# Kernel tuning notes

Measured on AMD Instinct MI355X. Metric: run time of the kernel, lower is better.

Reference implementation:

```python
import jax, jax.numpy as jnp
import numpy as np

B, S, H = 4, 2048, 576
NH, NKV, HD = 9, 3, 64
NEG = -1e9


def rotate_half(x):
    x1, x2 = x[..., : HD // 2], x[..., HD // 2 :]
    return jnp.concatenate((-x2, x1), axis=-1)


def setup_inputs() -> dict:
    key = jax.random.key(0)
    ks = jax.random.split(key, 6)
    x = jax.random.normal(ks[0], (B, S, H), dtype=jnp.float32)
    # realistic RoPE tables
    inv_freq = 1.0 / (10000.0 ** (np.arange(0, HD, 2, dtype=np.float32) / HD))
    pos = np.arange(S, dtype=np.float32)
    freqs = np.outer(pos, inv_freq)            # [S, HD//2]
    emb = np.concatenate([freqs, freqs], -1)   # [S, HD]
    cos = jnp.asarray(np.cos(emb), dtype=jnp.float32)
    sin = jnp.asarray(np.sin(emb), dtype=jnp.float32)
    # causal additive mask [1,1,S,S]
    causal = jnp.tril(jnp.ones((S, S), dtype=jnp.bool_))
    mask = jnp.where(causal, 0.0, NEG).astype(jnp.float32)[None, None]
    sc = 1.0 / np.sqrt(H)
    Wq = jax.random.normal(ks[1], (H, NH * HD), dtype=jnp.float32) * sc
    Wk = jax.random.normal(ks[2], (H, NKV * HD), dtype=jnp.float32) * sc
    Wv = jax.random.normal(ks[3], (H, NKV * HD), dtype=jnp.float32) * sc
    Wo = jax.random.normal(ks[4], (NH * HD, H), dtype=jnp.float32) * sc
    return {"x": x, "cos": cos, "sin": sin, "mask": mask,
            "Wq": Wq, "Wk": Wk, "Wv": Wv, "Wo": Wo}


def reference(x, cos, sin, mask, Wq, Wk, Wv, Wo):
    b, s, _ = x.shape
    # projections -> [b, heads, s, hd]
    q = (x @ Wq).reshape(b, s, NH, HD).transpose(0, 2, 1, 3)
    k = (x @ Wk).reshape(b, s, NKV, HD).transpose(0, 2, 1, 3)
    v = (x @ Wv).reshape(b, s, NKV, HD).transpose(0, 2, 1, 3)
    c = cos[None, None]  # [1,1,s,hd]
    sn = sin[None, None]
    q = q * c + rotate_half(q) * sn
    k = k * c + rotate_half(k) * sn
    # GQA: repeat_interleave KV heads to match query heads
    groups = NH // NKV
    k = jnp.repeat(k, groups, axis=1)
    v = jnp.repeat(v, groups, axis=1)
    scores = jnp.einsum("bhqd,bhkd->bhqk", q, k) / np.sqrt(HD)
    scores = scores + mask
    probs = jax.nn.softmax(scores, axis=-1)
    out = jnp.einsum("bhqk,bhkd->bhqd", probs, v)
    out = out.transpose(0, 2, 1, 3).reshape(b, s, NH * HD)
    return out @ Wo
```

## Files before the change

### kernel.cpp

```cpp
#include <hip/hip_runtime.h>
#include <math.h>

typedef __attribute__((ext_vector_type(4))) float f32x4;
typedef __attribute__((ext_vector_type(8))) short short8;
typedef __attribute__((ext_vector_type(8))) __bf16 bf16x8;
typedef __attribute__((ext_vector_type(2))) __bf16 bf16x2;
typedef __attribute__((ext_vector_type(2))) unsigned uint32x2;

#define NB 4
#define NS 2048
#define NHID 576
#define NHEADS 9
#define NKVH 3
#define NHD 64
#define NM (NB * NS)
#define NQKV 960
#define NGRP 3
#define QSC 0.18033688f

static __device__ __forceinline__ unsigned short f2bf(float f) {
  union { float f; unsigned u; } v; v.f = f;
  unsigned r = v.u + 0x7FFFu + ((v.u >> 16) & 1u);
  return (unsigned short)(r >> 16);
}
static __device__ __forceinline__ unsigned pk2bf(float a, float b) {
  bf16x2 h;
  h.x = (__bf16)a;
  h.y = (__bf16)b;
  return __builtin_bit_cast(unsigned, h);
}
static __device__ __forceinline__ f32x4 mfma16(short8 a, short8 b, f32x4 c) {
  return __builtin_amdgcn_mfma_f32_16x16x32_bf16(
      __builtin_bit_cast(bf16x8, a), __builtin_bit_cast(bf16x8, b), c, 0, 0, 0);
}
static __device__ __forceinline__ void gload16(const void* g, void* l) {
  __builtin_amdgcn_global_load_lds(
      (const __attribute__((address_space(1))) void*)g,
      (__attribute__((address_space(3))) void*)l, 16, 0, 0);
}

__global__ __launch_bounds__(256)
void k_cvt(const float* __restrict__ src, unsigned short* __restrict__ dst, const int n8) {
  const int t = blockIdx.x * 256 + threadIdx.x;
  if (t >= n8) return;
  const f32x4* sp = (const f32x4*)(src + (size_t)t * 8);
  f32x4 a = sp[0], b = sp[1];
  union { short8 v; unsigned short u[8]; } o;
#pragma unroll
  for (int e = 0; e < 4; ++e) { o.u[e] = f2bf(a[e]); o.u[4 + e] = f2bf(b[e]); }
  *(short8*)(dst + (size_t)t * 8) = o.v;
}

__global__ __launch_bounds__(256)
void k_transpose_cvt(const float* __restrict__ src, unsigned short* __restrict__ dst,
                     const int R, const int C) {
  __shared__ unsigned short tile[64 * 72];
  const int t = threadIdx.x;
  const int r0 = blockIdx.y * 64, c0 = blockIdx.x * 64;
  {
    const int rl = t >> 2, cb = (t & 3) * 16;
    const float* sp = src + (size_t)(r0 + rl) * C + c0 + cb;
#pragma unroll
    for (int jj = 0; jj < 4; ++jj) {
      f32x4 v = *(const f32x4*)(sp + jj * 4);
#pragma unroll
      for (int e = 0; e < 4; ++e) tile[rl * 72 + cb + jj * 4 + e] = f2bf(v[e]);
    }
  }
  __syncthreads();
  {
    const int cl = t >> 2, rb = (t & 3) * 16;
    union { short8 v; unsigned short u[8]; } o0, o1;
#pragma unroll
    for (int jj = 0; jj < 8; ++jj) {
      o0.u[jj] = tile[(rb + jj) * 72 + cl];
      o1.u[jj] = tile[(rb + 8 + jj) * 72 + cl];
    }
    unsigned short* dp = dst + (size_t)(c0 + cl) * R + r0 + rb;
    *(short8*)dp = o0.v;
    *(short8*)(dp + 8) = o1.v;
  }
}

template <int MODE>
__global__ __launch_bounds__(256)
void k_gemm_bt(const unsigned short* __restrict__ A,
               const unsigned short* __restrict__ Bt,
               void* __restrict__ Cv,
               const float* __restrict__ cosT,
               const float* __restrict__ sinT,
               const int M, const int N, const int K) {
  __shared__ unsigned short a_lds[2][128 * 64];
  __shared__ unsigned short b_lds[2][128 * 64];
  const int tid = threadIdx.x;
  const int w = tid >> 6, l = tid & 63, g = l >> 4, c = l & 15;
  const int tm = blockIdx.y * 128, tn = blockIdx.x * 128;
  const int wm = w >> 1, wn = w & 1;
  f32x4 acc[4][4] = {};
  const int nk = K >> 6;

#define GSTAGE(k0, half)                                                   \
  {                                                                        \
    _Pragma("unroll")                                                      \
    for (int q = 0; q < 4; ++q) {                                          \
      const int o = q * 4096 + w * 1024 + l * 16;                          \
      const int row = o >> 7;                                              \
      const int wb = (o & 127) ^ ((row & 7) << 4);                         \
      gload16(A + (size_t)(tm + row) * K + (k0) + (wb >> 1),               \
              (void*)(a_lds[half] + ((q * 4096 + w * 1024) >> 1)));        \
      gload16(Bt + (size_t)(tn + row) * K + (k0) + (wb >> 1),              \
              (void*)(b_lds[half] + ((q * 4096 + w * 1024) >> 1)));        \
    }                                                                      \
  }

  GSTAGE(0, 0);

  for (int k = 0; k < nk; ++k) {
    if (k + 1 < nk) {
      GSTAGE((k + 1) << 6, (k + 1) & 1);
      asm volatile("s_waitcnt vmcnt(8)" ::: "memory");
    } else {
      asm volatile("s_waitcnt vmcnt(0)" ::: "memory");
    }
    __builtin_amdgcn_s_barrier();
    __builtin_amdgcn_sched_barrier(0);
    const char* al = (const char*)a_lds[k & 1];
    const char* bl = (const char*)b_lds[k & 1];
#pragma unroll
    for (int dc = 0; dc < 2; ++dc) {
      short8 af[4], bf[4];
#pragma unroll
      for (int mt = 0; mt < 4; ++mt) {
        const int row = wm * 64 + mt * 16 + c;
        const int byt = ((row << 7) + (dc << 6) + (g << 4)) ^ ((row & 7) << 4);
        af[mt] = *(const short8*)(al + byt);
      }
#pragma unroll
      for (int nt = 0; nt < 4; ++nt) {
        const int row = wn * 64 + nt * 16 + c;
        const int byt = ((row << 7) + (dc << 6) + (g << 4)) ^ ((row & 7) << 4);
        bf[nt] = *(const short8*)(bl + byt);
      }
      __builtin_amdgcn_s_setprio(1);
#pragma unroll
      for (int mt = 0; mt < 4; ++mt)
#pragma unroll
        for (int nt = 0; nt < 4; ++nt)
          acc[mt][nt] = mfma16(af[mt], bf[nt], acc[mt][nt]);
      __builtin_amdgcn_s_setprio(0);
    }
    __builtin_amdgcn_sched_barrier(0);
    __builtin_amdgcn_s_barrier();
  }
#undef GSTAGE

  if (MODE == 1) {
#pragma unroll
    for (int mt = 0; mt < 4; ++mt)
#pragma unroll
      for (int nt = 0; nt < 4; ++nt) {
        const int cc = tn + wn * 64 + nt * 16 + c;
        if (cc < N) {
#pragma unroll
          for (int i = 0; i < 4; ++i) {
            const size_t rr = (size_t)(tm + wm * 64 + mt * 16 + 4 * g + i);
            ((float*)Cv)[rr * N + cc] = acc[mt][nt][i];
          }
        }
      }
  } else if (tn < 768) {
    const float qs = (tn + wn * 64) < 576 ? QSC : 1.0f;
    unsigned short* Cp = (unsigned short*)Cv;
#pragma unroll
    for (int mt = 0; mt < 4; ++mt)
#pragma unroll
      for (int i = 0; i < 4; ++i) {
        const int rr = tm + wm * 64 + mt * 16 + 4 * g + i;
        const int s = rr & (NS - 1);
        const float* cb = cosT + (size_t)s * NHD;
        const float* sb = sinT + (size_t)s * NHD;
#pragma unroll
        for (int p = 0; p < 2; ++p) {
          const float cn = cb[p * 16 + c];
          const float sn = sb[p * 16 + c];
          const float lo = acc[mt][p][i];
          const float hi = acc[mt][p + 2][i];
          const size_t base = (size_t)rr * N + tn + wn * 64 + p * 16 + c;
          Cp[base] = f2bf((lo * cn - hi * sn) * qs);
          Cp[base + 32] = f2bf((hi * cn + lo * sn) * qs);
        }
      }
  } else {
    unsigned short* Cp = (unsigned short*)Cv;
#pragma unroll
    for (int mt = 0; mt < 4; ++mt)
#pragma unroll
      for (int nt = 0; nt < 4; ++nt) {
        const int cc = tn + wn * 64 + nt * 16 + c;
        if (cc < N) {
#pragma unroll
          for (int i = 0; i < 4; ++i) {
            const size_t rr = (size_t)(tm + wm * 64 + mt * 16 + 4 * g + i);
            Cp[rr * N + cc] = f2bf(acc[mt][nt][i]);
          }
        }
      }
  }
}

__global__ __launch_bounds__(256)
void k_vt(const unsigned short* __restrict__ qkv, unsigned short* __restrict__ vt) {
  __shared__ unsigned short tile[64 * 72];
  const int t = threadIdx.x;
  const int st = blockIdx.x;
  const int by = blockIdx.y;
  const int b = by / NKVH, kh = by - b * NKVH;
  {
    const int sl2 = t >> 2, d0 = (t & 3) * 16;
    const unsigned short* sp = qkv + (size_t)(b * NS + st * 64 + sl2) * NQKV +
                               (NHEADS + NKVH) * NHD + kh * NHD + d0;
    *(short8*)&tile[sl2 * 72 + d0] = *(const short8*)sp;
    *(short8*)&tile[sl2 * 72 + d0 + 8] = *(const short8*)(sp + 8);
  }
  __syncthreads();
  {
    const int dl = t >> 2, s0 = (t & 3) * 16;
    union { short8 v; unsigned short u[8]; } o0, o1;
#pragma unroll
    for (int jj = 0; jj < 8; ++jj) {
      o0.u[jj] = tile[(s0 + jj) * 72 + dl];
      o1.u[jj] = tile[(s0 + 8 + jj) * 72 + dl];
    }
    unsigned short* dp = vt + (size_t)(by * 64 + dl) * NS + st * 64 + s0;
    *(short8*)dp = o0.v;
    *(short8*)(dp + 8) = o1.v;
  }
}

__global__ __launch_bounds__(256)
void k_attn(const unsigned short* __restrict__ qkv,
            const unsigned short* __restrict__ vt,
            unsigned short* __restrict__ ao) {
  __shared__ unsigned short kv_s[2][2][4096];
  __shared__ unsigned short p_s[4][1024];
  const int tid = threadIdx.x;
  const int w = tid >> 6, l = tid & 63, g = l >> 4, c = l & 15;
  const int bh = blockIdx.x;
  const int qt = 31 - (int)blockIdx.y;
  const int b = bh / NHEADS, h = bh - b * NHEADS, kh = h / NGRP;

  const char* kgb = (const char*)(qkv + (size_t)b * NS * NQKV + NHEADS * NHD + kh * NHD);
  const char* vgb = (const char*)(vt + (size_t)(b * NKVH + kh) * NHD * NS);

  const int lr = l >> 3;
  const int swz = ((l & 7) ^ lr) << 4;
  const int r0 = 16 * w + lr;
  const int cs = (c & 7) << 4;

  const size_t qrow = (size_t)(b * NS + qt * 64 + w * 16 + c) * NQKV + h * NHD;
  const short8 qf0 = *(const short8*)(qkv + qrow + g * 8);
  const short8 qf1 = *(const short8*)(qkv + qrow + 32 + g * 8);

  const short8 ones = {0x3F80, 0x3F80, 0x3F80, 0x3F80, 0x3F80, 0x3F80, 0x3F80, 0x3F80};

  f32x4 ot[4] = {};
  f32x4 lacc = {};
  float m = -1e30f;
  const int q_g = qt * 64 + w * 16 + c;

#define STAGE(j, half)                                                          \
  {                                                                             \
    unsigned short* kl_ = kv_s[half][0];                                        \
    unsigned short* vl_ = kv_s[half][1];                                        \
    gload16(kgb + (size_t)((j) * 64 + r0) * (NQKV * 2) + swz, kl_ + 16 * w * 64);       \
    gload16(kgb + (size_t)((j) * 64 + r0 + 8) * (NQKV * 2) + swz, kl_ + (16 * w + 8) * 64); \
    gload16(vgb + (size_t)r0 * (NS * 2) + (j) * 128 + swz, vl_ + 16 * w * 64);          \
    gload16(vgb + (size_t)(r0 + 8) * (NS * 2) + (j) * 128 + swz, vl_ + (16 * w + 8) * 64); \
  }

  STAGE(0, 0);

  for (int j = 0; j <= qt; ++j) {
    if (j < qt) {
      STAGE(j + 1, (j + 1) & 1);
      asm volatile("s_waitcnt vmcnt(4)" ::: "memory");
    } else {
      asm volatile("s_waitcnt vmcnt(0)" ::: "memory");
    }
    __builtin_amdgcn_s_barrier();
    __builtin_amdgcn_sched_barrier(0);
    const char* kl = (const char*)kv_s[j & 1][0];
    const char* vl = (const char*)kv_s[j & 1][1];

    f32x4 st[4] = {};
#pragma unroll
    for (int dc = 0; dc < 2; ++dc) {
      const int col = (dc * 64 + g * 16) ^ cs;
      const short8 qf = dc ? qf1 : qf0;
#pragma unroll
      for (int nt = 0; nt < 4; ++nt) {
        short8 kf = *(const short8*)(kl + (nt * 16 + c) * 128 + col);
        st[nt] = mfma16(kf, qf, st[nt]);
      }
    }

    if (j == qt) {
#pragma unroll
      for (int nt = 0; nt < 4; ++nt)
#pragma unroll
        for (int i = 0; i < 4; ++i) {
          const int kvg = j * 64 + nt * 16 + 4 * g + i;
          if (kvg > q_g) st[nt][i] = -1e30f;
        }
    }

    float m0 = fmaxf(fmaxf(st[0][0], st[0][1]), st[0][2]);
    float m1 = fmaxf(fmaxf(st[0][3], st[1][0]), st[1][1]);
    float m2 = fmaxf(fmaxf(st[1][2], st[1][3]), st[2][0]);
    float m3 = fmaxf(fmaxf(st[2][1], st[2][2]), st[2][3]);
    float m4 = fmaxf(fmaxf(st[3][0], st[3][1]), st[3][2]);
    float pm = fmaxf(fmaxf(fmaxf(m0, m1), fmaxf(m2, m3)), fmaxf(m4, st[3][3]));
    pm = fmaxf(pm, __shfl_xor(pm, 16));
    pm = fmaxf(pm, __shfl_xor(pm, 32));

    if (!__all(pm <= m + 8.0f)) {
      const float scl = exp2f(m - pm);
      m = pm;
      lacc *= scl;
#pragma unroll
      for (int nt = 0; nt < 4; ++nt) ot[nt] *= scl;
    }

    {
      char* pw = (char*)p_s[w];
#pragma unroll
      for (int nt = 0; nt < 4; ++nt) {
        float p0 = exp2f(st[nt][0] - m);
        float p1 = exp2f(st[nt][1] - m);
        float p2 = exp2f(st[nt][2] - m);
        float p3 = exp2f(st[nt][3] - m);
        uint32x2 pk;
        pk.x = pk2bf(p0, p1);
        pk.y = pk2bf(p2, p3);
        *(uint32x2*)(pw + c * 128 + ((nt * 32 + g * 8) ^ cs)) = pk;
      }
#pragma unroll
      for (int dc = 0; dc < 2; ++dc) {
        const int col = (dc * 64 + g * 16) ^ cs;
        short8 pf = *(const short8*)(pw + c * 128 + col);
        lacc = mfma16(ones, pf, lacc);
#pragma unroll
        for (int nt = 0; nt < 4; ++nt) {
          short8 vf = *(const short8*)(vl + (nt * 16 + c) * 128 + col);
          ot[nt] = mfma16(vf, pf, ot[nt]);
        }
      }
    }
    __builtin_amdgcn_sched_barrier(0);
    __builtin_amdgcn_s_barrier();
  }

  {
    char* ol = (char*)kv_s[0][0];
    const float inv = __builtin_amdgcn_rcpf(lacc[0]);
#pragma unroll
    for (int nt = 0; nt < 4; ++nt) {
      uint32x2 pk;
      pk.x = pk2bf(ot[nt][0] * inv, ot[nt][1] * inv);
      pk.y = pk2bf(ot[nt][2] * inv, ot[nt][3] * inv);
      *(uint32x2*)(ol + (w * 16 + c) * 128 + ((nt * 32 + g * 8) ^ cs)) = pk;
    }
  }
  __syncthreads();
  {
    const char* ol = (const char*)kv_s[0][0];
    const int rr = tid >> 2, cb = tid & 3;
    const int rk = (rr & 7) << 4;
    short8 v0 = *(const short8*)(ol + rr * 128 + ((cb * 32) ^ rk));
    short8 v1 = *(const short8*)(ol + rr * 128 + ((cb * 32 + 16) ^ rk));
    char* aop = (char*)(ao + (size_t)(b * NS + qt * 64 + rr) * (NHEADS * NHD) + h * NHD + cb * 16);
    *(short8*)aop = v0;
    *(short8*)(aop + 16) = v1;
  }
#undef STAGE
}

extern "C" void kernel_launch(void* const* d_in, const int* in_sizes, int n_in,
                              void* d_out, int out_size, void* d_ws, size_t ws_size,
                              hipStream_t stream) {
  const float* x = (const float*)d_in[0];
  const float* cosT = (const float*)d_in[1];
  const float* sinT = (const float*)d_in[2];
  const float* Wq = (const float*)d_in[4];
  const float* Wk = (const float*)d_in[5];
  const float* Wv = (const float*)d_in[6];
  const float* Wo = (const float*)d_in[7];

  unsigned short* xb = (unsigned short*)d_ws;
  unsigned short* wqkvT = xb + (size_t)NM * NHID;
  unsigned short* woT = wqkvT + (size_t)NQKV * NHID;
  unsigned short* qkv = woT + (size_t)NHID * NHID;
  unsigned short* vt = qkv + (size_t)NM * NQKV;
  unsigned short* ao = vt + (size_t)NB * NKVH * NHD * NS;

  k_cvt<<<dim3((NM * NHID / 8 + 255) / 256), 256, 0, stream>>>(x, xb, NM * NHID / 8);
  k_transpose_cvt<<<dim3(9, 9), 256, 0, stream>>>(Wq, wqkvT, NHID, NHID);
  k_transpose_cvt<<<dim3(3, 9), 256, 0, stream>>>(Wk, wqkvT + (size_t)576 * 576, NHID, 192);
  k_transpose_cvt<<<dim3(3, 9), 256, 0, stream>>>(Wv, wqkvT + (size_t)768 * 576, NHID, 192);
  k_transpose_cvt<<<dim3(9, 9), 256, 0, stream>>>(Wo, woT, NHID, NHID);
  k_gemm_bt<0><<<dim3((NQKV + 127) / 128, NM / 128), 256, 0, stream>>>(
      xb, wqkvT, (void*)qkv, cosT, sinT, NM, NQKV, NHID);
  k_vt<<<dim3(NS / 64, NB * NKVH), 256, 0, stream>>>(qkv, vt);
  k_attn<<<dim3(NB * NHEADS, NS / 64), 256, 0, stream>>>(qkv, vt, ao);
  k_gemm_bt<1><<<dim3((NHID + 127) / 128, NM / 128), 256, 0, stream>>>(
      ao, woT, d_out, nullptr, nullptr, NM, NHID, NHID);
}
```

Before: 106.0 us.

## Split long causal query tiles into two KV chunks and fuse V transpose into GEMM

The QKV GEMM epilogue now writes V directly in transposed layout, which removes the separate k_vt transpose kernel and shrinks the qkv row stride to 768. The attention grid is extended to 48 tiles per head. The 16 longest query tiles are split into two KV ranges whose unnormalised partial outputs and (m, l) statistics go to a workspace, and a new combine kernel merges them. The aim is to balance the causal workload across CUs and cut one launch and one pass over V, at the cost of an extra kernel, extra partial-result traffic, and bf16 rounding of the partial outputs.

```diff
diff --git a/kernel.cpp b/kernel.cpp
--- a/kernel.cpp
+++ b/kernel.cpp
@@ -15,6 +15,7 @@
 #define NHD 64
 #define NM (NB * NS)
 #define NQKV 960
+#define QKS 768
 #define NGRP 3
 #define QSC 0.18033688f
 
@@ -28,6 +29,10 @@
   h.x = (__bf16)a;
   h.y = (__bf16)b;
   return __builtin_bit_cast(unsigned, h);
+}
+static __device__ __forceinline__ float bf2f(unsigned short h) {
+  union { unsigned u; float f; } v; v.u = ((unsigned)h) << 16;
+  return v.f;
 }
 static __device__ __forceinline__ f32x4 mfma16(short8 a, short8 b, f32x4 c) {
   return __builtin_amdgcn_mfma_f32_16x16x32_bf16(
@@ -87,6 +92,7 @@
 void k_gemm_bt(const unsigned short* __restrict__ A,
                const unsigned short* __restrict__ Bt,
                void* __restrict__ Cv,
+               unsigned short* __restrict__ vtb,
                const float* __restrict__ cosT,
                const float* __restrict__ sinT,
                const int M, const int N, const int K) {
@@ -185,71 +191,50 @@
           const float sn = sb[p * 16 + c];
           const float lo = acc[mt][p][i];
           const float hi = acc[mt][p + 2][i];
-          const size_t base = (size_t)rr * N + tn + wn * 64 + p * 16 + c;
+          const size_t base = (size_t)rr * QKS + tn + wn * 64 + p * 16 + c;
           Cp[base] = f2bf((lo * cn - hi * sn) * qs);
           Cp[base + 32] = f2bf((hi * cn + lo * sn) * qs);
         }
       }
   } else {
-    unsigned short* Cp = (unsigned short*)Cv;
 #pragma unroll
     for (int mt = 0; mt < 4; ++mt)
 #pragma unroll
       for (int nt = 0; nt < 4; ++nt) {
         const int cc = tn + wn * 64 + nt * 16 + c;
-        if (cc < N) {
-#pragma unroll
-          for (int i = 0; i < 4; ++i) {
-            const size_t rr = (size_t)(tm + wm * 64 + mt * 16 + 4 * g + i);
-            Cp[rr * N + cc] = f2bf(acc[mt][nt][i]);
-          }
+        if (cc < 960) {
+          const int rr0 = tm + wm * 64 + mt * 16 + 4 * g;
+          const int bb = rr0 >> 11, ss = rr0 & (NS - 1);
+          const int grp = bb * NKVH + ((cc - 768) >> 6);
+          const int d = (cc - 768) & 63;
+          uint32x2 pk;
+          pk.x = pk2bf(acc[mt][nt][0], acc[mt][nt][1]);
+          pk.y = pk2bf(acc[mt][nt][2], acc[mt][nt][3]);
+          *(uint32x2*)(vtb + (size_t)grp * (NHD * NS) + (size_t)d * NS + ss) = pk;
         }
       }
-  }
-}
-
-__global__ __launch_bounds__(256)
-void k_vt(const unsigned short* __restrict__ qkv, unsigned short* __restrict__ vt) {
-  __shared__ unsigned short tile[64 * 72];
-  const int t = threadIdx.x;
-  const int st = blockIdx.x;
-  const int by = blockIdx.y;
-  const int b = by / NKVH, kh = by - b * NKVH;
-  {
-    const int sl2 = t >> 2, d0 = (t & 3) * 16;
-    const unsigned short* sp = qkv + (size_t)(b * NS + st * 64 + sl2) * NQKV +
-                               (NHEADS + NKVH) * NHD + kh * NHD + d0;
-    *(short8*)&tile[sl2 * 72 + d0] = *(const short8*)sp;
-    *(short8*)&tile[sl2 * 72 + d0 + 8] = *(const short8*)(sp + 8);
-  }
-  __syncthreads();
-  {
-    const int dl = t >> 2, s0 = (t & 3) * 16;
-    union { short8 v; unsigned short u[8]; } o0, o1;
-#pragma unroll
-    for (int jj = 0; jj < 8; ++jj) {
-      o0.u[jj] = tile[(s0 + jj) * 72 + dl];
-      o1.u[jj] = tile[(s0 + 8 + jj) * 72 + dl];
-    }
-    unsigned short* dp = vt + (size_t)(by * 64 + dl) * NS + st * 64 + s0;
-    *(short8*)dp = o0.v;
-    *(short8*)(dp + 8) = o1.v;
   }
 }
 
 __global__ __launch_bounds__(256)
 void k_attn(const unsigned short* __restrict__ qkv,
             const unsigned short* __restrict__ vt,
-            unsigned short* __restrict__ ao) {
+            unsigned short* __restrict__ ao,
+            unsigned short* __restrict__ pO,
+            float* __restrict__ pML) {
   __shared__ unsigned short kv_s[2][2][4096];
   __shared__ unsigned short p_s[4][1024];
   const int tid = threadIdx.x;
   const int w = tid >> 6, l = tid & 63, g = l >> 4, c = l & 15;
   const int bh = blockIdx.x;
-  const int qt = 31 - (int)blockIdx.y;
+  const int y = blockIdx.y;
+  int qt, j0, j1, ch, partial;
+  if (y < 16) { qt = 16 + y; j0 = 0; j1 = 16; ch = 0; partial = 1; }
+  else if (y < 32) { qt = 47 - y; j0 = 16; j1 = qt + 1; ch = 1; partial = 1; }
+  else { qt = 47 - y; j0 = 0; j1 = qt + 1; ch = 0; partial = 0; }
   const int b = bh / NHEADS, h = bh - b * NHEADS, kh = h / NGRP;
 
-  const char* kgb = (const char*)(qkv + (size_t)b * NS * NQKV + NHEADS * NHD + kh * NHD);
+  const char* kgb = (const char*)(qkv + (size_t)b * NS * QKS + NHEADS * NHD + kh * NHD);
   const char* vgb = (const char*)(vt + (size_t)(b * NKVH + kh) * NHD * NS);
 
   const int lr = l >> 3;
@@ -257,7 +242,7 @@
   const int r0 = 16 * w + lr;
   const int cs = (c & 7) << 4;
 
-  const size_t qrow = (size_t)(b * NS + qt * 64 + w * 16 + c) * NQKV + h * NHD;
+  const size_t qrow = (size_t)(b * NS + qt * 64 + w * 16 + c) * QKS + h * NHD;
   const short8 qf0 = *(const short8*)(qkv + qrow + g * 8);
   const short8 qf1 = *(const short8*)(qkv + qrow + 32 + g * 8);
 
@@ -272,16 +257,16 @@
   {                                                                             \
     unsigned short* kl_ = kv_s[half][0];                                        \
     unsigned short* vl_ = kv_s[half][1];                                        \
-    gload16(kgb + (size_t)((j) * 64 + r0) * (NQKV * 2) + swz, kl_ + 16 * w * 64);       \
-    gload16(kgb + (size_t)((j) * 64 + r0 + 8) * (NQKV * 2) + swz, kl_ + (16 * w + 8) * 64); \
+    gload16(kgb + (size_t)((j) * 64 + r0) * (QKS * 2) + swz, kl_ + 16 * w * 64);        \
+    gload16(kgb + (size_t)((j) * 64 + r0 + 8) * (QKS * 2) + swz, kl_ + (16 * w + 8) * 64); \
     gload16(vgb + (size_t)r0 * (NS * 2) + (j) * 128 + swz, vl_ + 16 * w * 64);          \
     gload16(vgb + (size_t)(r0 + 8) * (NS * 2) + (j) * 128 + swz, vl_ + (16 * w + 8) * 64); \
   }
 
-  STAGE(0, 0);
-
-  for (int j = 0; j <= qt; ++j) {
-    if (j < qt) {
+  STAGE(j0, j0 & 1);
+
+  for (int j = j0; j < j1; ++j) {
+    if (j + 1 < j1) {
       STAGE(j + 1, (j + 1) & 1);
       asm volatile("s_waitcnt vmcnt(4)" ::: "memory");
     } else {
@@ -359,30 +344,81 @@
     __builtin_amdgcn_sched_barrier(0);
     __builtin_amdgcn_s_barrier();
   }
-
-  {
-    char* ol = (char*)kv_s[0][0];
-    const float inv = __builtin_amdgcn_rcpf(lacc[0]);
+#undef STAGE
+
+  if (partial) {
+    const int pidx = (bh * 16 + (qt - 16)) * 2 + ch;
+    unsigned short* po = pO + (size_t)pidx * 4096;
 #pragma unroll
     for (int nt = 0; nt < 4; ++nt) {
       uint32x2 pk;
-      pk.x = pk2bf(ot[nt][0] * inv, ot[nt][1] * inv);
-      pk.y = pk2bf(ot[nt][2] * inv, ot[nt][3] * inv);
-      *(uint32x2*)(ol + (w * 16 + c) * 128 + ((nt * 32 + g * 8) ^ cs)) = pk;
-    }
-  }
-  __syncthreads();
-  {
-    const char* ol = (const char*)kv_s[0][0];
-    const int rr = tid >> 2, cb = tid & 3;
-    const int rk = (rr & 7) << 4;
-    short8 v0 = *(const short8*)(ol + rr * 128 + ((cb * 32) ^ rk));
-    short8 v1 = *(const short8*)(ol + rr * 128 + ((cb * 32 + 16) ^ rk));
-    char* aop = (char*)(ao + (size_t)(b * NS + qt * 64 + rr) * (NHEADS * NHD) + h * NHD + cb * 16);
-    *(short8*)aop = v0;
-    *(short8*)(aop + 16) = v1;
-  }
-#undef STAGE
+      pk.x = pk2bf(ot[nt][0], ot[nt][1]);
+      pk.y = pk2bf(ot[nt][2], ot[nt][3]);
+      *(uint32x2*)(po + (w * 16 + c) * 64 + nt * 16 + 4 * g) = pk;
+    }
+    if (g == 0) {
+      float* ml = pML + (size_t)pidx * 128;
+      ml[w * 16 + c] = m;
+      ml[64 + w * 16 + c] = lacc[0];
+    }
+  } else {
+    {
+      char* ol = (char*)kv_s[0][0];
+      const float inv = __builtin_amdgcn_rcpf(lacc[0]);
+#pragma unroll
+      for (int nt = 0; nt < 4; ++nt) {
+        uint32x2 pk;
+        pk.x = pk2bf(ot[nt][0] * inv, ot[nt][1] * inv);
+        pk.y = pk2bf(ot[nt][2] * inv, ot[nt][3] * inv);
+        *(uint32x2*)(ol + (w * 16 + c) * 128 + ((nt * 32 + g * 8) ^ cs)) = pk;
+      }
+    }
+    __syncthreads();
+    {
+      const char* ol = (const char*)kv_s[0][0];
+      const int rr = tid >> 2, cb = tid & 3;
+      const int rk = (rr & 7) << 4;
+      short8 v0 = *(const short8*)(ol + rr * 128 + ((cb * 32) ^ rk));
+      short8 v1 = *(const short8*)(ol + rr * 128 + ((cb * 32 + 16) ^ rk));
+      char* aop = (char*)(ao + (size_t)(b * NS + qt * 64 + rr) * NHID + h * NHD + cb * 16);
+      *(short8*)aop = v0;
+      *(short8*)(aop + 16) = v1;
+    }
+  }
+}
+
+__global__ __launch_bounds__(256)
+void k_comb(const unsigned short* __restrict__ pO, const float* __restrict__ pML,
+            unsigned short* __restrict__ ao) {
+  const int bh = blockIdx.x, qte = blockIdx.y;
+  const int b = bh / NHEADS, h = bh - b * NHEADS;
+  const int t = threadIdx.x;
+  const int q = t >> 2, dg = t & 3;
+  const int pidx = (bh * 16 + qte) * 2;
+  const float* ml1 = pML + (size_t)pidx * 128;
+  const float* ml2 = ml1 + 128;
+  const float m1 = ml1[q], l1 = ml1[64 + q];
+  const float m2 = ml2[q], l2 = ml2[64 + q];
+  const float M = fmaxf(m1, m2);
+  const float s1 = exp2f(m1 - M), s2 = exp2f(m2 - M);
+  const float inv = __builtin_amdgcn_rcpf(l1 * s1 + l2 * s2);
+  const unsigned short* o1 = pO + (size_t)pidx * 4096 + q * 64 + dg * 16;
+  const unsigned short* o2 = o1 + 4096;
+  short8 a0 = *(const short8*)o1, a1 = *(const short8*)(o1 + 8);
+  short8 b0 = *(const short8*)o2, b1 = *(const short8*)(o2 + 8);
+  union { unsigned u[4]; short8 v; } r0, r1;
+#pragma unroll
+  for (int k = 0; k < 4; ++k) {
+    float x0 = (bf2f((unsigned short)a0[2 * k]) * s1 + bf2f((unsigned short)b0[2 * k]) * s2) * inv;
+    float x1 = (bf2f((unsigned short)a0[2 * k + 1]) * s1 + bf2f((unsigned short)b0[2 * k + 1]) * s2) * inv;
+    r0.u[k] = pk2bf(x0, x1);
+    float y0 = (bf2f((unsigned short)a1[2 * k]) * s1 + bf2f((unsigned short)b1[2 * k]) * s2) * inv;
+    float y1 = (bf2f((unsigned short)a1[2 * k + 1]) * s1 + bf2f((unsigned short)b1[2 * k + 1]) * s2) * inv;
+    r1.u[k] = pk2bf(y0, y1);
+  }
+  unsigned short* dst = ao + (size_t)(b * NS + (16 + qte) * 64 + q) * NHID + h * NHD + dg * 16;
+  *(short8*)dst = r0.v;
+  *(short8*)(dst + 8) = r1.v;
 }
 
 extern "C" void kernel_launch(void* const* d_in, const int* in_sizes, int n_in,
@@ -400,8 +436,10 @@
   unsigned short* wqkvT = xb + (size_t)NM * NHID;
   unsigned short* woT = wqkvT + (size_t)NQKV * NHID;
   unsigned short* qkv = woT + (size_t)NHID * NHID;
-  unsigned short* vt = qkv + (size_t)NM * NQKV;
-  unsigned short* ao = vt + (size_t)NB * NKVH * NHD * NS;
+  unsigned short* vt = qkv + (size_t)NM * QKS;
+  unsigned short* pO = vt + (size_t)NB * NKVH * NHD * NS;
+  float* pML = (float*)(pO + (size_t)36 * 16 * 2 * 4096);
+  unsigned short* ao = xb;
 
   k_cvt<<<dim3((NM * NHID / 8 + 255) / 256), 256, 0, stream>>>(x, xb, NM * NHID / 8);
   k_transpose_cvt<<<dim3(9, 9), 256, 0, stream>>>(Wq, wqkvT, NHID, NHID);
@@ -409,9 +447,9 @@
   k_transpose_cvt<<<dim3(3, 9), 256, 0, stream>>>(Wv, wqkvT + (size_t)768 * 576, NHID, 192);
   k_transpose_cvt<<<dim3(9, 9), 256, 0, stream>>>(Wo, woT, NHID, NHID);
   k_gemm_bt<0><<<dim3((NQKV + 127) / 128, NM / 128), 256, 0, stream>>>(
-      xb, wqkvT, (void*)qkv, cosT, sinT, NM, NQKV, NHID);
-  k_vt<<<dim3(NS / 64, NB * NKVH), 256, 0, stream>>>(qkv, vt);
-  k_attn<<<dim3(NB * NHEADS, NS / 64), 256, 0, stream>>>(qkv, vt, ao);
+      xb, wqkvT, (void*)qkv, vt, cosT, sinT, NM, NQKV, NHID);
+  k_attn<<<dim3(NB * NHEADS, 48), 256, 0, stream>>>(qkv, vt, ao, pO, pML);
+  k_comb<<<dim3(NB * NHEADS, 16), 256, 0, stream>>>(pO, pML, ao);
   k_gemm_bt<1><<<dim3((NHID + 127) / 128, NM / 128), 256, 0, stream>>>(
-      ao, woT, d_out, nullptr, nullptr, NM, NHID, NHID);
-}
+      ao, woT, d_out, nullptr, nullptr, nullptr, NM, NHID, NHID);
+}
```

Result: slower. 111.8 us (+5.5%).

## Fuse V transpose into QKV GEMM epilogue and double-buffer attention loop statically

Applied to the files above, without the earlier changes.

The QKV GEMM epilogue now writes the V columns straight into the transposed [b,kvh,d,s] layout, so the separate k_vt transpose kernel and its launch are gone. Q/K now live in a narrower 768-wide buffer, and the attention output reuses the x bf16 buffer. The attention main loop is unrolled by two with fixed LDS buffer indices and incrementing load pointers, which cuts per-iteration address arithmetic. In exchange, the GEMM epilogue issues strided 8-byte stores for V, and aliasing ao onto xb relies on xb being dead once the QKV GEMM has finished.

```diff
diff --git a/kernel.cpp b/kernel.cpp
--- a/kernel.cpp
+++ b/kernel.cpp
@@ -15,6 +15,7 @@
 #define NHD 64
 #define NM (NB * NS)
 #define NQKV 960
+#define QKS 768
 #define NGRP 3
 #define QSC 0.18033688f
 
@@ -28,6 +29,10 @@
   h.x = (__bf16)a;
   h.y = (__bf16)b;
   return __builtin_bit_cast(unsigned, h);
+}
+static __device__ __forceinline__ float bf2f(unsigned short h) {
+  union { unsigned u; float f; } v; v.u = ((unsigned)h) << 16;
+  return v.f;
 }
 static __device__ __forceinline__ f32x4 mfma16(short8 a, short8 b, f32x4 c) {
   return __builtin_amdgcn_mfma_f32_16x16x32_bf16(
@@ -87,6 +92,7 @@
 void k_gemm_bt(const unsigned short* __restrict__ A,
                const unsigned short* __restrict__ Bt,
                void* __restrict__ Cv,
+               unsigned short* __restrict__ vtb,
                const float* __restrict__ cosT,
                const float* __restrict__ sinT,
                const int M, const int N, const int K) {
@@ -185,55 +191,28 @@
           const float sn = sb[p * 16 + c];
           const float lo = acc[mt][p][i];
           const float hi = acc[mt][p + 2][i];
-          const size_t base = (size_t)rr * N + tn + wn * 64 + p * 16 + c;
+          const size_t base = (size_t)rr * QKS + tn + wn * 64 + p * 16 + c;
           Cp[base] = f2bf((lo * cn - hi * sn) * qs);
           Cp[base + 32] = f2bf((hi * cn + lo * sn) * qs);
         }
       }
   } else {
-    unsigned short* Cp = (unsigned short*)Cv;
 #pragma unroll
     for (int mt = 0; mt < 4; ++mt)
 #pragma unroll
       for (int nt = 0; nt < 4; ++nt) {
         const int cc = tn + wn * 64 + nt * 16 + c;
-        if (cc < N) {
-#pragma unroll
-          for (int i = 0; i < 4; ++i) {
-            const size_t rr = (size_t)(tm + wm * 64 + mt * 16 + 4 * g + i);
-            Cp[rr * N + cc] = f2bf(acc[mt][nt][i]);
-          }
+        if (cc < 960) {
+          const int rr0 = tm + wm * 64 + mt * 16 + 4 * g;
+          const int bb = rr0 >> 11, ss = rr0 & (NS - 1);
+          const int grp = bb * NKVH + ((cc - 768) >> 6);
+          const int d = (cc - 768) & 63;
+          uint32x2 pk;
+          pk.x = pk2bf(acc[mt][nt][0], acc[mt][nt][1]);
+          pk.y = pk2bf(acc[mt][nt][2], acc[mt][nt][3]);
+          *(uint32x2*)(vtb + (size_t)grp * (NHD * NS) + (size_t)d * NS + ss) = pk;
         }
       }
-  }
-}
-
-__global__ __launch_bounds__(256)
-void k_vt(const unsigned short* __restrict__ qkv, unsigned short* __restrict__ vt) {
-  __shared__ unsigned short tile[64 * 72];
-  const int t = threadIdx.x;
-  const int st = blockIdx.x;
-  const int by = blockIdx.y;
-  const int b = by / NKVH, kh = by - b * NKVH;
-  {
-    const int sl2 = t >> 2, d0 = (t & 3) * 16;
-    const unsigned short* sp = qkv + (size_t)(b * NS + st * 64 + sl2) * NQKV +
-                               (NHEADS + NKVH) * NHD + kh * NHD + d0;
-    *(short8*)&tile[sl2 * 72 + d0] = *(const short8*)sp;
-    *(short8*)&tile[sl2 * 72 + d0 + 8] = *(const short8*)(sp + 8);
-  }
-  __syncthreads();
-  {
-    const int dl = t >> 2, s0 = (t & 3) * 16;
-    union { short8 v; unsigned short u[8]; } o0, o1;
-#pragma unroll
-    for (int jj = 0; jj < 8; ++jj) {
-      o0.u[jj] = tile[(s0 + jj) * 72 + dl];
-      o1.u[jj] = tile[(s0 + 8 + jj) * 72 + dl];
-    }
-    unsigned short* dp = vt + (size_t)(by * 64 + dl) * NS + st * 64 + s0;
-    *(short8*)dp = o0.v;
-    *(short8*)(dp + 8) = o1.v;
   }
 }
 
@@ -249,15 +228,19 @@
   const int qt = 31 - (int)blockIdx.y;
   const int b = bh / NHEADS, h = bh - b * NHEADS, kh = h / NGRP;
 
-  const char* kgb = (const char*)(qkv + (size_t)b * NS * NQKV + NHEADS * NHD + kh * NHD);
-  const char* vgb = (const char*)(vt + (size_t)(b * NKVH + kh) * NHD * NS);
-
   const int lr = l >> 3;
   const int swz = ((l & 7) ^ lr) << 4;
   const int r0 = 16 * w + lr;
   const int cs = (c & 7) << 4;
 
-  const size_t qrow = (size_t)(b * NS + qt * 64 + w * 16 + c) * NQKV + h * NHD;
+  const char* kp0 = (const char*)(qkv + (size_t)b * NS * QKS + NHEADS * NHD + kh * NHD) +
+                    (size_t)r0 * (QKS * 2) + swz;
+  const char* kp1 = kp0 + 8 * (QKS * 2);
+  const char* vp0 = (const char*)(vt + (size_t)(b * NKVH + kh) * NHD * NS) +
+                    (size_t)r0 * (NS * 2) + swz;
+  const char* vp1 = vp0 + 8 * (NS * 2);
+
+  const size_t qrow = (size_t)(b * NS + qt * 64 + w * 16 + c) * QKS + h * NHD;
   const short8 qf0 = *(const short8*)(qkv + qrow + g * 8);
   const short8 qf1 = *(const short8*)(qkv + qrow + 32 + g * 8);
 
@@ -268,97 +251,111 @@
   float m = -1e30f;
   const int q_g = qt * 64 + w * 16 + c;
 
-#define STAGE(j, half)                                                          \
+#define STAGE(BUF)                                                \
+  {                                                               \
+    gload16(kp0, kv_s[BUF][0] + 16 * w * 64);                     \
+    gload16(kp1, kv_s[BUF][0] + (16 * w + 8) * 64);               \
+    gload16(vp0, kv_s[BUF][1] + 16 * w * 64);                     \
+    gload16(vp1, kv_s[BUF][1] + (16 * w + 8) * 64);               \
+    kp0 += 64 * (QKS * 2); kp1 += 64 * (QKS * 2);                 \
+    vp0 += 128; vp1 += 128;                                       \
+  }
+
+#define COMPUTE(BUF, jj)                                                        \
   {                                                                             \
-    unsigned short* kl_ = kv_s[half][0];                                        \
-    unsigned short* vl_ = kv_s[half][1];                                        \
-    gload16(kgb + (size_t)((j) * 64 + r0) * (NQKV * 2) + swz, kl_ + 16 * w * 64);       \
-    gload16(kgb + (size_t)((j) * 64 + r0 + 8) * (NQKV * 2) + swz, kl_ + (16 * w + 8) * 64); \
-    gload16(vgb + (size_t)r0 * (NS * 2) + (j) * 128 + swz, vl_ + 16 * w * 64);          \
-    gload16(vgb + (size_t)(r0 + 8) * (NS * 2) + (j) * 128 + swz, vl_ + (16 * w + 8) * 64); \
-  }
-
-  STAGE(0, 0);
-
-  for (int j = 0; j <= qt; ++j) {
+    const char* kl = (const char*)kv_s[BUF][0];                                 \
+    const char* vl = (const char*)kv_s[BUF][1];                                 \
+    f32x4 st[4] = {};                                                           \
+    _Pragma("unroll")                                                           \
+    for (int dc = 0; dc < 2; ++dc) {                                            \
+      const int col = (dc * 64 + g * 16) ^ cs;                                  \
+      const short8 qf = dc ? qf1 : qf0;                                         \
+      _Pragma("unroll")                                                         \
+      for (int nt = 0; nt < 4; ++nt) {                                          \
+        short8 kf = *(const short8*)(kl + (nt * 16 + c) * 128 + col);           \
+        st[nt] = mfma16(kf, qf, st[nt]);                                        \
+      }                                                                         \
+    }                                                                           \
+    if ((jj) == qt) {                                                           \
+      _Pragma("unroll")                                                         \
+      for (int nt = 0; nt < 4; ++nt)                                            \
+        _Pragma("unroll")                                                       \
+        for (int i = 0; i < 4; ++i) {                                           \
+          const int kvg = (jj) * 64 + nt * 16 + 4 * g + i;                      \
+          if (kvg > q_g) st[nt][i] = -1e30f;                                    \
+        }                                                                       \
+    }                                                                           \
+    float m0 = fmaxf(fmaxf(st[0][0], st[0][1]), st[0][2]);                      \
+    float m1 = fmaxf(fmaxf(st[0][3], st[1][0]), st[1][1]);                      \
+    float m2 = fmaxf(fmaxf(st[1][2], st[1][3]), st[2][0]);                      \
+    float m3 = fmaxf(fmaxf(st[2][1], st[2][2]), st[2][3]);                      \
+    float m4 = fmaxf(fmaxf(st[3][0], st[3][1]), st[3][2]);                      \
+    float pm = fmaxf(fmaxf(fmaxf(m0, m1), fmaxf(m2, m3)), fmaxf(m4, st[3][3]));\
+    pm = fmaxf(pm, __shfl_xor(pm, 16));                                         \
+    pm = fmaxf(pm, __shfl_xor(pm, 32));                                         \
+    if (!__all(pm <= m + 8.0f)) {                                               \
+      const float scl = exp2f(m - pm);                                          \
+      m = pm;                                                                   \
+      lacc *= scl;                                                              \
+      _Pragma("unroll")                                                         \
+      for (int nt = 0; nt < 4; ++nt) ot[nt] *= scl;                             \
+    }                                                                           \
+    {                                                                           \
+      char* pw = (char*)p_s[w];                                                 \
+      _Pragma("unroll")                                                         \
+      for (int nt = 0; nt < 4; ++nt) {                                          \
+        float p0 = exp2f(st[nt][0] - m);                                        \
+        float p1 = exp2f(st[nt][1] - m);                                        \
+        float p2 = exp2f(st[nt][2] - m);                                        \
+        float p3 = exp2f(st[nt][3] - m);                                        \
+        uint32x2 pk;                                                            \
+        pk.x = pk2bf(p0, p1);                                                   \
+        pk.y = pk2bf(p2, p3);                                                   \
+        *(uint32x2*)(pw + c * 128 + ((nt * 32 + g * 8) ^ cs)) = pk;             \
+      }                                                                         \
+      _Pragma("unroll")                                                         \
+      for (int dc = 0; dc < 2; ++dc) {                                          \
+        const int col = (dc * 64 + g * 16) ^ cs;                                \
+        short8 pf = *(const short8*)(pw + c * 128 + col);                       \
+        lacc = mfma16(ones, pf, lacc);                                          \
+        _Pragma("unroll")                                                       \
+        for (int nt = 0; nt < 4; ++nt) {                                        \
+          short8 vf = *(const short8*)(vl + (nt * 16 + c) * 128 + col);         \
+          ot[nt] = mfma16(vf, pf, ot[nt]);                                      \
+        }                                                                       \
+      }                                                                         \
+    }                                                                           \
+  }
+
+  STAGE(0);
+
+  for (int j = 0; j <= qt; j += 2) {
     if (j < qt) {
-      STAGE(j + 1, (j + 1) & 1);
+      STAGE(1);
       asm volatile("s_waitcnt vmcnt(4)" ::: "memory");
     } else {
       asm volatile("s_waitcnt vmcnt(0)" ::: "memory");
     }
     __builtin_amdgcn_s_barrier();
     __builtin_amdgcn_sched_barrier(0);
-    const char* kl = (const char*)kv_s[j & 1][0];
-    const char* vl = (const char*)kv_s[j & 1][1];
-
-    f32x4 st[4] = {};
-#pragma unroll
-    for (int dc = 0; dc < 2; ++dc) {
-      const int col = (dc * 64 + g * 16) ^ cs;
-      const short8 qf = dc ? qf1 : qf0;
-#pragma unroll
-      for (int nt = 0; nt < 4; ++nt) {
-        short8 kf = *(const short8*)(kl + (nt * 16 + c) * 128 + col);
-        st[nt] = mfma16(kf, qf, st[nt]);
-      }
-    }
-
-    if (j == qt) {
-#pragma unroll
-      for (int nt = 0; nt < 4; ++nt)
-#pragma unroll
-        for (int i = 0; i < 4; ++i) {
-          const int kvg = j * 64 + nt * 16 + 4 * g + i;
-          if (kvg > q_g) st[nt][i] = -1e30f;
-        }
-    }
-
-    float m0 = fmaxf(fmaxf(st[0][0], st[0][1]), st[0][2]);
-    float m1 = fmaxf(fmaxf(st[0][3], st[1][0]), st[1][1]);
-    float m2 = fmaxf(fmaxf(st[1][2], st[1][3]), st[2][0]);
-    float m3 = fmaxf(fmaxf(st[2][1], st[2][2]), st[2][3]);
-    float m4 = fmaxf(fmaxf(st[3][0], st[3][1]), st[3][2]);
-    float pm = fmaxf(fmaxf(fmaxf(m0, m1), fmaxf(m2, m3)), fmaxf(m4, st[3][3]));
-    pm = fmaxf(pm, __shfl_xor(pm, 16));
-    pm = fmaxf(pm, __shfl_xor(pm, 32));
-
-    if (!__all(pm <= m + 8.0f)) {
-      const float scl = exp2f(m - pm);
-      m = pm;
-      lacc *= scl;
-#pragma unroll
-      for (int nt = 0; nt < 4; ++nt) ot[nt] *= scl;
-    }
-
-    {
-      char* pw = (char*)p_s[w];
-#pragma unroll
-      for (int nt = 0; nt < 4; ++nt) {
-        float p0 = exp2f(st[nt][0] - m);
-        float p1 = exp2f(st[nt][1] - m);
-        float p2 = exp2f(st[nt][2] - m);
-        float p3 = exp2f(st[nt][3] - m);
-        uint32x2 pk;
-        pk.x = pk2bf(p0, p1);
-        pk.y = pk2bf(p2, p3);
-        *(uint32x2*)(pw + c * 128 + ((nt * 32 + g * 8) ^ cs)) = pk;
-      }
-#pragma unroll
-      for (int dc = 0; dc < 2; ++dc) {
-        const int col = (dc * 64 + g * 16) ^ cs;
-        short8 pf = *(const short8*)(pw + c * 128 + col);
-        lacc = mfma16(ones, pf, lacc);
-#pragma unroll
-        for (int nt = 0; nt < 4; ++nt) {
-          short8 vf = *(const short8*)(vl + (nt * 16 + c) * 128 + col);
-          ot[nt] = mfma16(vf, pf, ot[nt]);
-        }
-      }
-    }
-    __builtin_amdgcn_sched_barrier(0);
-    __builtin_amdgcn_s_barrier();
-  }
+    COMPUTE(0, j);
+    __builtin_amdgcn_sched_barrier(0);
+    __builtin_amdgcn_s_barrier();
+    if (j + 1 > qt) break;
+    if (j + 1 < qt) {
+      STAGE(0);
+      asm volatile("s_waitcnt vmcnt(4)" ::: "memory");
+    } else {
+      asm volatile("s_waitcnt vmcnt(0)" ::: "memory");
+    }
+    __builtin_amdgcn_s_barrier();
+    __builtin_amdgcn_sched_barrier(0);
+    COMPUTE(1, j + 1);
+    __builtin_amdgcn_sched_barrier(0);
+    __builtin_amdgcn_s_barrier();
+  }
+#undef STAGE
+#undef COMPUTE
 
   {
     char* ol = (char*)kv_s[0][0];
@@ -378,11 +375,10 @@
     const int rk = (rr & 7) << 4;
     short8 v0 = *(const short8*)(ol + rr * 128 + ((cb * 32) ^ rk));
     short8 v1 = *(const short8*)(ol + rr * 128 + ((cb * 32 + 16) ^ rk));
-    char* aop = (char*)(ao + (size_t)(b * NS + qt * 64 + rr) * (NHEADS * NHD) + h * NHD + cb * 16);
+    char* aop = (char*)(ao + (size_t)(b * NS + qt * 64 + rr) * NHID + h * NHD + cb * 16);
     *(short8*)aop = v0;
     *(short8*)(aop + 16) = v1;
   }
-#undef STAGE
 }
 
 extern "C" void kernel_launch(void* const* d_in, const int* in_sizes, int n_in,
@@ -400,8 +396,8 @@
   unsigned short* wqkvT = xb + (size_t)NM * NHID;
   unsigned short* woT = wqkvT + (size_t)NQKV * NHID;
   unsigned short* qkv = woT + (size_t)NHID * NHID;
-  unsigned short* vt = qkv + (size_t)NM * NQKV;
-  unsigned short* ao = vt + (size_t)NB * NKVH * NHD * NS;
+  unsigned short* vt = qkv + (size_t)NM * QKS;
+  unsigned short* ao = xb;
 
   k_cvt<<<dim3((NM * NHID / 8 + 255) / 256), 256, 0, stream>>>(x, xb, NM * NHID / 8);
   k_transpose_cvt<<<dim3(9, 9), 256, 0, stream>>>(Wq, wqkvT, NHID, NHID);
@@ -409,9 +405,8 @@
   k_transpose_cvt<<<dim3(3, 9), 256, 0, stream>>>(Wv, wqkvT + (size_t)768 * 576, NHID, 192);
   k_transpose_cvt<<<dim3(9, 9), 256, 0, stream>>>(Wo, woT, NHID, NHID);
   k_gemm_bt<0><<<dim3((NQKV + 127) / 128, NM / 128), 256, 0, stream>>>(
-      xb, wqkvT, (void*)qkv, cosT, sinT, NM, NQKV, NHID);
-  k_vt<<<dim3(NS / 64, NB * NKVH), 256, 0, stream>>>(qkv, vt);
+      xb, wqkvT, (void*)qkv, vt, cosT, sinT, NM, NQKV, NHID);
   k_attn<<<dim3(NB * NHEADS, NS / 64), 256, 0, stream>>>(qkv, vt, ao);
   k_gemm_bt<1><<<dim3((NHID + 127) / 128, NM / 128), 256, 0, stream>>>(
-      ao, woT, d_out, nullptr, nullptr, NM, NHID, NHID);
-}
+      ao, woT, d_out, nullptr, nullptr, nullptr, NM, NHID, NHID);
+}
```

Result: faster. 103.4 us (-2.5%).
